# Optimization experiments

Measured on AMD Instinct MI355X. Metric: run time of the kernel, lower is better.

Reference implementation:

```python
import jax, jax.numpy as jnp
import numpy as np

S, B, H = 2048, 2, 2048
NH = 16
HD = H // NH  # 128
ROPE_BASE = 10000.0


def _rope_cos_sin(seq_len, dim, dtype):
    inv_freq = 1.0 / (ROPE_BASE ** (jnp.arange(0, dim, 2, dtype=jnp.float32) / dim))
    t = jnp.arange(seq_len, dtype=jnp.float32)
    freqs = jnp.outer(t, inv_freq)            # [S, dim/2]
    emb = jnp.concatenate([freqs, freqs], -1)  # [S, dim]
    return jnp.cos(emb).astype(dtype), jnp.sin(emb).astype(dtype)


def _rotate_half(x):
    x1, x2 = jnp.split(x, 2, axis=-1)
    return jnp.concatenate([-x2, x1], axis=-1)


def setup_inputs() -> dict:
    key = jax.random.key(0)
    k1, k2, k3 = jax.random.split(key, 3)
    hidden_states = jax.random.normal(k1, (S, B, H), dtype=jnp.float32)
    w_qkv = jax.random.normal(k2, (3 * H, H), dtype=jnp.float32) * (1.0 / np.sqrt(H))
    w_out = jax.random.normal(k3, (H, H), dtype=jnp.float32) * (1.0 / np.sqrt(H))
    return {"hidden_states": hidden_states, "w_qkv": w_qkv, "w_out": w_out}


def reference(hidden_states, w_qkv, w_out):
    seq_len, batch, _ = hidden_states.shape
    # QKV projection (nn.Linear: x @ W^T), bias=False
    qkv = jnp.einsum('sbh,oh->sbo', hidden_states, w_qkv)
    qkv = qkv.reshape(seq_len, batch, 3, NH, HD)
    q, k, v = qkv[:, :, 0], qkv[:, :, 1], qkv[:, :, 2]  # [S, B, NH, HD]

    cos, sin = _rope_cos_sin(seq_len, HD, hidden_states.dtype)
    cos = cos[:, None, None, :]
    sin = sin[:, None, None, :]
    q = q * cos + _rotate_half(q) * sin
    k = k * cos + _rotate_half(k) * sin

    # [S, B, NH, HD] -> [B, NH, S, HD]
    q = q.transpose(1, 2, 0, 3)
    k = k.transpose(1, 2, 0, 3)
    v = v.transpose(1, 2, 0, 3)

    scale = 1.0 / np.sqrt(HD)
    scores = jnp.einsum('bhqd,bhkd->bhqk', q, k) * scale
    causal = jnp.tril(jnp.ones((seq_len, seq_len), dtype=bool))
    scores = jnp.where(causal, scores, jnp.finfo(scores.dtype).min)
    probs = jax.nn.softmax(scores, axis=-1)
    attn = jnp.einsum('bhqk,bhkd->bhqd', probs, v)  # [B, NH, S, HD]

    # [B, NH, S, HD] -> [S, B, NH*HD]
    out = attn.transpose(2, 0, 1, 3).reshape(seq_len, batch, -1)
    out = jnp.einsum('sbh,oh->sbo', out, w_out)
    return out
```

## Files before the change

### kernel.cpp

```cpp
#include <hip/hip_runtime.h>
#include <hip/hip_bf16.h>

typedef __attribute__((ext_vector_type(8))) short bf16x8;
typedef __attribute__((ext_vector_type(8))) short s16x8;
typedef __attribute__((ext_vector_type(4))) float f32x4;
typedef __attribute__((ext_vector_type(4))) int i32x4;
typedef __attribute__((ext_vector_type(2))) unsigned u32x2;

#define SEQ 2048
#define BATCH 2
#define HID 2048
#define NH 16
#define HD 128
#define QKVN 6144
#define QKN 4096

static __device__ __forceinline__ short f2bf(float f) {
    union { float f; unsigned u; } v; v.f = f;
    unsigned r = (v.u + 0x7FFFu + ((v.u >> 16) & 1u)) >> 16;
    return (short)r;
}

static __device__ __forceinline__ void gload_lds16(const short* g, short* l) {
    __builtin_amdgcn_global_load_lds((const __attribute__((address_space(1))) void*)g,
                                     (__attribute__((address_space(3))) void*)l, 16, 0, 0);
}

static __device__ __forceinline__ void cvt_body(const float* in, short* out, int i) {
    f32x4 a = *(const f32x4*)(in + (size_t)i * 8);
    f32x4 b = *(const f32x4*)(in + (size_t)i * 8 + 4);
    s16x8 o = { f2bf(a.x), f2bf(a.y), f2bf(a.z), f2bf(a.w),
                f2bf(b.x), f2bf(b.y), f2bf(b.z), f2bf(b.w) };
    *(s16x8*)(out + (size_t)i * 8) = o;
}

__global__ void cvt_kernel(const float* __restrict__ in, short* __restrict__ out, int n8) {
    const int i = blockIdx.x * 256 + threadIdx.x;
    if (i >= n8) return;
    cvt_body(in, out, i);
}

__global__ void cvt2_kernel(const float* __restrict__ inA, short* __restrict__ outA,
                            const float* __restrict__ inB, short* __restrict__ outB) {
    const int bid = blockIdx.x;
    if (bid < 4096) cvt_body(inA, outA, bid * 256 + threadIdx.x);
    else            cvt_body(inB, outB, (bid - 4096) * 256 + threadIdx.x);
}

#define G128_STAGE_A(BUF, HA, KK) do { \
    const short* _s = ((HA) ? aS1 : aS0) + (size_t)(KK) * 64; \
    short* _d = lds + (BUF) * 16384 + (HA) * 8192 + w * 512; \
    gload_lds16(_s, _d); \
    gload_lds16(_s + (size_t)128 * K, _d + 4096); \
} while (0)

#define G128_STAGE_B(BUF, HB, KK) do { \
    const short* _s = ((HB) ? bS1 : bS0) + (size_t)(KK) * 64; \
    short* _d = lds + 32768 + (BUF) * 8192 + (HB) * 4096 + w * 512; \
    gload_lds16(_s, _d); \
} while (0)

#define G128_LOAD_A(HA) do { \
    const short* _p = lds + bufR * 16384 + (HA) * 8192; \
    _Pragma("unroll") \
    for (int mm = 0; mm < 2; ++mm) { \
        aR[mm][0] = *(const bf16x8*)(_p + aOff0 + mm * 1024); \
        aR[mm][1] = *(const bf16x8*)(_p + aOff1 + mm * 1024); \
    } \
} while (0)

#define G128_LOAD_B(HB) do { \
    const short* _p = lds + 32768 + bufR * 8192 + (HB) * 4096; \
    _Pragma("unroll") \
    for (int nn = 0; nn < 2; ++nn) { \
        bR[(HB) * 2 + nn][0] = *(const bf16x8*)(_p + bOff0 + nn * 2048); \
        bR[(HB) * 2 + nn][1] = *(const bf16x8*)(_p + bOff1 + nn * 2048); \
    } \
} while (0)

#define G128_MFMA(HA, HB) do { \
    _Pragma("unroll") \
    for (int mm = 0; mm < 2; ++mm) { \
        _Pragma("unroll") \
        for (int nn = 0; nn < 2; ++nn) { \
            f32x4 _c = acc[(HA) * 2 + mm][(HB) * 2 + nn]; \
            _c = __builtin_amdgcn_mfma_f32_16x16x32_bf16(aR[mm][0], bR[(HB) * 2 + nn][0], _c, 0, 0, 0); \
            _c = __builtin_amdgcn_mfma_f32_16x16x32_bf16(aR[mm][1], bR[(HB) * 2 + nn][1], _c, 0, 0, 0); \
            acc[(HA) * 2 + mm][(HB) * 2 + nn] = _c; \
        } \
    } \
} while (0)

template<int MODE>
__global__ __launch_bounds__(512, 2)
void gemm128n(const short* __restrict__ A, const short* __restrict__ B,
              void* __restrict__ Cp, short* __restrict__ vTp, int N, int K) {
    __shared__ short lds[49152];

    const int tid = threadIdx.x;
    const int mBase = blockIdx.y * 256;
    const int nBase = blockIdx.x * 128;
    const int w = tid >> 6, lane = tid & 63, quad = lane >> 4, l15 = lane & 15;
    const int wm = w >> 1, wn = w & 1;

    const int kcol = 8 * ((tid & 7) ^ ((tid >> 3) & 7));
    const int srow = ((tid >> 3) & 15) + (tid >> 7) * 32;
    const short* aS0 = A + (size_t)(mBase + srow) * K + kcol;
    const short* aS1 = aS0 + (size_t)16 * K;
    const short* bS0 = B + (size_t)(nBase + srow) * K + kcol;
    const short* bS1 = bS0 + (size_t)16 * K;

    const int cs0 = (quad * 8) ^ ((l15 & 7) << 3);
    const int aOff0 = (l15 + wm * 32) * 64 + cs0;
    const int aOff1 = aOff0 ^ 32;
    const int bOff0 = (l15 + wn * 16) * 64 + cs0;
    const int bOff1 = bOff0 ^ 32;

    const int NK = K >> 6;
    f32x4 acc[4][4] = {};
    bf16x8 aR[2][2], bR[4][2];

    G128_STAGE_A(0, 0, 0); G128_STAGE_B(0, 0, 0); G128_STAGE_B(0, 1, 0); G128_STAGE_A(0, 1, 0);
    G128_STAGE_A(1, 0, 1); G128_STAGE_B(1, 0, 1); G128_STAGE_B(1, 1, 1);
    asm volatile("s_waitcnt vmcnt(4)" ::: "memory");
    __builtin_amdgcn_s_barrier();

    int bufR = 0;
    for (int k = 0; k < NK; ++k) {
        const int kk1 = (k + 1 < NK) ? k + 1 : NK - 1;
        const int kk2 = (k + 2 < NK) ? k + 2 : NK - 1;
        G128_LOAD_A(0);
        G128_LOAD_B(0);
        G128_STAGE_A(bufR ^ 1, 1, kk1);
        asm volatile("s_waitcnt lgkmcnt(4)" ::: "memory");
        __builtin_amdgcn_s_barrier();
        asm volatile("s_waitcnt lgkmcnt(0)" ::: "memory");
        __builtin_amdgcn_s_setprio(1);
        G128_MFMA(0, 0);
        __builtin_amdgcn_s_setprio(0);
        __builtin_amdgcn_s_barrier();
        G128_LOAD_B(1);
        G128_STAGE_A(bufR, 0, kk2);
        __builtin_amdgcn_s_barrier();
        asm volatile("s_waitcnt lgkmcnt(0)" ::: "memory");
        __builtin_amdgcn_s_setprio(1);
        G128_MFMA(0, 1);
        __builtin_amdgcn_s_setprio(0);
        __builtin_amdgcn_s_barrier();
        G128_LOAD_A(1);
        G128_STAGE_B(bufR, 0, kk2);
        __builtin_amdgcn_s_barrier();
        asm volatile("s_waitcnt lgkmcnt(0)" ::: "memory");
        __builtin_amdgcn_s_setprio(1);
        G128_MFMA(1, 1);
        __builtin_amdgcn_s_setprio(0);
        __builtin_amdgcn_s_barrier();
        G128_STAGE_B(bufR, 1, kk2);
        asm volatile("s_waitcnt vmcnt(4)" ::: "memory");
        __builtin_amdgcn_s_barrier();
        __builtin_amdgcn_s_setprio(1);
        G128_MFMA(1, 0);
        __builtin_amdgcn_s_setprio(0);
        __builtin_amdgcn_s_barrier();
        bufR ^= 1;
    }
    asm volatile("s_waitcnt vmcnt(0)" ::: "memory");

    if (MODE == 1 && nBase < 4096) {
        const float post = (nBase < 2048) ? 0.08838834764831845f : 1.0f;
        short* C = (short*)Cp;
        #pragma unroll
        for (int af = 0; af < 4; ++af) {
            const int ha = af >> 1, mm = af & 1;
            const int row0 = mBase + wm * 64 + (2 * mm + ha) * 16 + quad * 4;
            #pragma unroll
            for (int hb = 0; hb < 2; ++hb) {
                const int d = wn * 32 + hb * 16 + l15;
                const float inv_freq =
                    __expf(-((float)(2 * d) * (1.0f / 128.0f)) * 9.210340371976184f);
                #pragma unroll
                for (int rp = 0; rp < 2; ++rp) {
                    const int s = (row0 >> 1) + rp;
                    float sn, cs;
                    __sincosf((float)s * inv_freq, &sn, &cs);
                    #pragma unroll
                    for (int rr = 0; rr < 2; ++rr) {
                        const int r = rp * 2 + rr;
                        const float x1 = acc[af][hb * 2 + 0][r];
                        const float x2 = acc[af][hb * 2 + 1][r];
                        const size_t rb = (size_t)(row0 + r) * QKN + nBase + d;
                        C[rb]      = f2bf((x1 * cs - x2 * sn) * post);
                        C[rb + 64] = f2bf((x2 * cs + x1 * sn) * post);
                    }
                }
            }
        }
    } else if (MODE == 1) {
        __builtin_amdgcn_s_barrier();
        #pragma unroll
        for (int af = 0; af < 4; ++af) {
            const int ha = af >> 1, mm = af & 1;
            const int rbase = wm * 64 + (2 * mm + ha) * 16 + quad * 4;
            #pragma unroll
            for (int bg = 0; bg < 4; ++bg) {
                const int hb = bg >> 1, nn = bg & 1;
                const int d = nn * 64 + wn * 32 + hb * 16 + l15;
                #pragma unroll
                for (int bb = 0; bb < 2; ++bb) {
                    const unsigned lo = (unsigned short)f2bf(acc[af][bg][bb]);
                    const unsigned hi = (unsigned short)f2bf(acc[af][bg][bb + 2]);
                    *(unsigned*)&lds[bb * 16896 + d * 132 + (rbase >> 1)] =
                        lo | (hi << 16);
                }
            }
        }
        __syncthreads();
        const int h = (nBase - 4096) >> 7;
        const int s0 = mBase >> 1;
        const int hw = tid >> 5, l5 = tid & 31;
        #pragma unroll
        for (int pass = 0; pass < 16; ++pass) {
            const int rho = pass * 16 + hw;
            const int bb = rho >> 7, dd = rho & 127;
            const u32x2 v2 = *(const u32x2*)&lds[bb * 16896 + dd * 132 + l5 * 4];
            *(u32x2*)&vTp[((size_t)(bb * 16 + h) * 128 + dd) * 2048 + s0 + l5 * 4] = v2;
        }
    } else {
        #pragma unroll
        for (int af = 0; af < 4; ++af) {
            const int ha = af >> 1, mm = af & 1;
            const int row0 = mBase + wm * 64 + (2 * mm + ha) * 16 + quad * 4;
            #pragma unroll
            for (int bg = 0; bg < 4; ++bg) {
                const int hb = bg >> 1, nn = bg & 1;
                const int col = nBase + nn * 64 + wn * 32 + hb * 16 + l15;
                #pragma unroll
                for (int r = 0; r < 4; ++r)
                    ((float*)Cp)[(size_t)(row0 + r) * N + col] = acc[af][bg][r];
            }
        }
    }
}

__global__ __launch_bounds__(256, 2)
void attn_kernel(const short* __restrict__ qkv, const short* __restrict__ vT,
                 short* __restrict__ out) {
    __shared__ short lds[40960];

    const int bx = blockIdx.x;
    const int h = blockIdx.y, b = blockIdx.z;
    const int Aq = (bx & 1) ? (bx >> 1) : (15 - (bx >> 1));
    const int qt = b ? (15 - Aq) : Aq;
    const int tid = threadIdx.x;
    const int w = tid >> 6, lane = tid & 63, quad = lane >> 4, l15 = lane & 15;
    const int bh = b * 16 + h;
    const int cswz = (l15 & 7) << 3;

    bf16x8 aq[2][4];
    #pragma unroll
    for (int m = 0; m < 2; ++m) {
        const short* qbase =
            qkv + (size_t)((qt * 128 + w * 32 + m * 16 + l15) * 2 + b) * QKN + h * 128;
        #pragma unroll
        for (int c = 0; c < 4; ++c)
            aq[m][c] = *(const bf16x8*)(qbase + c * 32 + quad * 8);
    }

    f32x4 oacc[2][8] = {};
    float lpart[2][4] = {};

    const short* kSrc0 = qkv + (size_t)((w * 16 + (lane >> 4)) * 2 + b) * QKN
                       + 2048 + h * 128 + ((lane & 15) ^ (lane >> 4)) * 8;
    const short* kSrc1 = qkv + (size_t)((w * 16 + 4 + (lane >> 4)) * 2 + b) * QKN
                       + 2048 + h * 128 + ((lane & 15) ^ (4 | (lane >> 4))) * 8;
    const short* vSrc = vT + ((size_t)bh * 128 + w * 32 + (lane >> 3)) * 2048
                      + ((lane & 7) ^ ((lane >> 3) & 7)) * 8;
    short* kDst = lds + w * 2048;
    short* vDst = lds + 16384 + w * 2048;

#define STAGE_KV(BUF, KK0) do { \
    const size_t kAdv = (size_t)(KK0) * 2 * QKN; \
    short* _kd = kDst + (BUF) * 8192; \
    short* _vd = vDst + (BUF) * 8192; \
    gload_lds16(kSrc0 + kAdv,                  _kd); \
    gload_lds16(kSrc1 + kAdv,                  _kd + 512); \
    gload_lds16(kSrc0 + kAdv + 16 * QKN,       _kd + 1024); \
    gload_lds16(kSrc1 + kAdv + 16 * QKN,       _kd + 1536); \
    gload_lds16(vSrc + (KK0),                  _vd); \
    gload_lds16(vSrc + (KK0) + 8 * 2048,       _vd + 512); \
    gload_lds16(vSrc + (KK0) + 16 * 2048,      _vd + 1024); \
    gload_lds16(vSrc + (KK0) + 24 * 2048,      _vd + 1536); \
} while (0)

    const int nChunks = 2 * qt + 2;

    STAGE_KV(0, 0);
    asm volatile("s_waitcnt vmcnt(0)" ::: "memory");
    __builtin_amdgcn_s_barrier();

    for (int ck = 0; ck < nChunks; ++ck) {
        const int cur = ck & 1;
        const int kk0 = ck * 64;
        if (ck + 1 < nChunks) STAGE_KV(cur ^ 1, kk0 + 64);

        const short* Kc = lds + cur * 8192;
        const short* Vc = lds + 16384 + cur * 8192;
        short* Pw = lds + 32768 + w * 2048;

        f32x4 sc4[2][4] = {};
        #pragma unroll
        for (int c = 0; c < 4; ++c) {
            const int cb = (c * 32 + quad * 8) ^ cswz;
            #pragma unroll
            for (int n = 0; n < 4; ++n) {
                bf16x8 bk = *(const bf16x8*)(Kc + (n * 16 + l15) * 128 + cb);
                sc4[0][n] = __builtin_amdgcn_mfma_f32_16x16x32_bf16(aq[0][c], bk, sc4[0][n], 0, 0, 0);
                sc4[1][n] = __builtin_amdgcn_mfma_f32_16x16x32_bf16(aq[1][c], bk, sc4[1][n], 0, 0, 0);
            }
        }

        const bool diag = (ck >= 2 * qt);
        #pragma unroll
        for (int m = 0; m < 2; ++m) {
            const int rowbase = qt * 128 + w * 32 + m * 16 + quad * 4;
            #pragma unroll
            for (int r = 0; r < 4; ++r) {
                const int prow = m * 16 + quad * 4 + r;
                const int pswz = ((quad * 4 + r) & 7) << 3;
                #pragma unroll
                for (int n = 0; n < 4; ++n) {
                    float sv = sc4[m][n][r];
                    if (diag && (kk0 + n * 16 + l15 > rowbase + r)) sv = -1e30f;
                    const float p = __expf(sv);
                    lpart[m][r] += p;
                    Pw[prow * 64 + ((n * 16 + l15) ^ pswz)] = f2bf(p);
                }
            }
        }

        #pragma unroll
        for (int kp2 = 0; kp2 < 2; ++kp2) {
            const int cb = (kp2 * 32 + quad * 8) ^ cswz;
            bf16x8 ap0 = *(const bf16x8*)(Pw + l15 * 64 + cb);
            bf16x8 ap1 = *(const bf16x8*)(Pw + (16 + l15) * 64 + cb);
            #pragma unroll
            for (int dt = 0; dt < 8; ++dt) {
                bf16x8 bv = *(const bf16x8*)(Vc + (dt * 16 + l15) * 64 + cb);
                oacc[0][dt] = __builtin_amdgcn_mfma_f32_16x16x32_bf16(ap0, bv, oacc[0][dt], 0, 0, 0);
                oacc[1][dt] = __builtin_amdgcn_mfma_f32_16x16x32_bf16(ap1, bv, oacc[1][dt], 0, 0, 0);
            }
        }

        asm volatile("s_waitcnt vmcnt(0)" ::: "memory");
        __builtin_amdgcn_s_barrier();
    }
#undef STAGE_KV

    #pragma unroll
    for (int m = 0; m < 2; ++m) {
        const int rowbase = qt * 128 + w * 32 + m * 16 + quad * 4;
        #pragma unroll
        for (int r = 0; r < 4; ++r) {
            float l = lpart[m][r];
            #pragma unroll
            for (int off = 1; off < 16; off <<= 1)
                l += __shfl_xor(l, off);
            const float inv_l = 1.0f / l;
            const size_t obase = (size_t)((rowbase + r) * 2 + b) * HID + h * 128;
            #pragma unroll
            for (int dt = 0; dt < 8; ++dt)
                out[obase + dt * 16 + l15] = f2bf(oacc[m][dt][r] * inv_l);
        }
    }
}

extern "C" void kernel_launch(void* const* d_in, const int* in_sizes, int n_in,
                              void* d_out, int out_size, void* d_ws, size_t ws_size,
                              hipStream_t stream) {
    const float* hidden = (const float*)d_in[0];
    const float* w_qkv  = (const float*)d_in[1];
    const float* w_out  = (const float*)d_in[2];
    float* out = (float*)d_out;

    short* qkv     = (short*)d_ws;
    short* attnb   = qkv + (size_t)4096 * QKN;
    short* wqkv_bf = attnb + (size_t)4096 * HID;
    short* wout_bf = wqkv_bf;
    short* hbf     = wqkv_bf + (size_t)QKVN * HID;
    short* vT      = hbf + (size_t)4096 * HID;

    dim3 blk(256);
    cvt2_kernel<<<dim3(4096 + 6144), blk, 0, stream>>>(hidden, hbf, w_qkv, wqkv_bf);
    gemm128n<1><<<dim3(QKVN / 128, 4096 / 256), dim3(512), 0, stream>>>(
        hbf, wqkv_bf, qkv, vT, QKVN, HID);
    cvt_kernel<<<dim3(2048), blk, 0, stream>>>(w_out, wout_bf, 2048 * 256);
    attn_kernel<<<dim3(SEQ / 128, NH, BATCH), blk, 0, stream>>>(qkv, vT, attnb);
    gemm128n<0><<<dim3(HID / 128, 4096 / 256), dim3(512), 0, stream>>>(
        attnb, wout_bf, out, nullptr, HID, HID);
}
```

Baseline: 345.8 us.

## Transpose QK^T MFMA operands, pack P stores, and pad QK row stride

```diff
diff --git a/kernel.cpp b/kernel.cpp
--- a/kernel.cpp
+++ b/kernel.cpp
@@ -13,7 +13,7 @@
 #define NH 16
 #define HD 128
 #define QKVN 6144
-#define QKN 4096
+#define QKS 4160
 
 static __device__ __forceinline__ short f2bf(float f) {
     union { float f; unsigned u; } v; v.f = f;
@@ -188,7 +188,7 @@
                         const int r = rp * 2 + rr;
                         const float x1 = acc[af][hb * 2 + 0][r];
                         const float x2 = acc[af][hb * 2 + 1][r];
-                        const size_t rb = (size_t)(row0 + r) * QKN + nBase + d;
+                        const size_t rb = (size_t)(row0 + r) * QKS + nBase + d;
                         C[rb]      = f2bf((x1 * cs - x2 * sn) * post);
                         C[rb + 64] = f2bf((x2 * cs + x1 * sn) * post);
                     }
@@ -260,18 +260,18 @@
     #pragma unroll
     for (int m = 0; m < 2; ++m) {
         const short* qbase =
-            qkv + (size_t)((qt * 128 + w * 32 + m * 16 + l15) * 2 + b) * QKN + h * 128;
+            qkv + (size_t)((qt * 128 + w * 32 + m * 16 + l15) * 2 + b) * QKS + h * 128;
         #pragma unroll
         for (int c = 0; c < 4; ++c)
             aq[m][c] = *(const bf16x8*)(qbase + c * 32 + quad * 8);
     }
 
     f32x4 oacc[2][8] = {};
-    float lpart[2][4] = {};
-
-    const short* kSrc0 = qkv + (size_t)((w * 16 + (lane >> 4)) * 2 + b) * QKN
+    float lpart[2] = {};
+
+    const short* kSrc0 = qkv + (size_t)((w * 16 + (lane >> 4)) * 2 + b) * QKS
                        + 2048 + h * 128 + ((lane & 15) ^ (lane >> 4)) * 8;
-    const short* kSrc1 = qkv + (size_t)((w * 16 + 4 + (lane >> 4)) * 2 + b) * QKN
+    const short* kSrc1 = qkv + (size_t)((w * 16 + 4 + (lane >> 4)) * 2 + b) * QKS
                        + 2048 + h * 128 + ((lane & 15) ^ (4 | (lane >> 4))) * 8;
     const short* vSrc = vT + ((size_t)bh * 128 + w * 32 + (lane >> 3)) * 2048
                       + ((lane & 7) ^ ((lane >> 3) & 7)) * 8;
@@ -279,13 +279,13 @@
     short* vDst = lds + 16384 + w * 2048;
 
 #define STAGE_KV(BUF, KK0) do { \
-    const size_t kAdv = (size_t)(KK0) * 2 * QKN; \
+    const size_t kAdv = (size_t)(KK0) * 2 * QKS; \
     short* _kd = kDst + (BUF) * 8192; \
     short* _vd = vDst + (BUF) * 8192; \
     gload_lds16(kSrc0 + kAdv,                  _kd); \
     gload_lds16(kSrc1 + kAdv,                  _kd + 512); \
-    gload_lds16(kSrc0 + kAdv + 16 * QKN,       _kd + 1024); \
-    gload_lds16(kSrc1 + kAdv + 16 * QKN,       _kd + 1536); \
+    gload_lds16(kSrc0 + kAdv + 16 * QKS,       _kd + 1024); \
+    gload_lds16(kSrc1 + kAdv + 16 * QKS,       _kd + 1536); \
     gload_lds16(vSrc + (KK0),                  _vd); \
     gload_lds16(vSrc + (KK0) + 8 * 2048,       _vd + 512); \
     gload_lds16(vSrc + (KK0) + 16 * 2048,      _vd + 1024); \
@@ -307,34 +307,40 @@
         const short* Vc = lds + 16384 + cur * 8192;
         short* Pw = lds + 32768 + w * 2048;
 
-        f32x4 sc4[2][4] = {};
+        f32x4 sc4[4][2] = {};
         #pragma unroll
         for (int c = 0; c < 4; ++c) {
             const int cb = (c * 32 + quad * 8) ^ cswz;
             #pragma unroll
-            for (int n = 0; n < 4; ++n) {
-                bf16x8 bk = *(const bf16x8*)(Kc + (n * 16 + l15) * 128 + cb);
-                sc4[0][n] = __builtin_amdgcn_mfma_f32_16x16x32_bf16(aq[0][c], bk, sc4[0][n], 0, 0, 0);
-                sc4[1][n] = __builtin_amdgcn_mfma_f32_16x16x32_bf16(aq[1][c], bk, sc4[1][n], 0, 0, 0);
+            for (int kc = 0; kc < 4; ++kc) {
+                bf16x8 ak = *(const bf16x8*)(Kc + (kc * 16 + l15) * 128 + cb);
+                sc4[kc][0] = __builtin_amdgcn_mfma_f32_16x16x32_bf16(ak, aq[0][c], sc4[kc][0], 0, 0, 0);
+                sc4[kc][1] = __builtin_amdgcn_mfma_f32_16x16x32_bf16(ak, aq[1][c], sc4[kc][1], 0, 0, 0);
             }
         }
 
         const bool diag = (ck >= 2 * qt);
-        #pragma unroll
-        for (int m = 0; m < 2; ++m) {
-            const int rowbase = qt * 128 + w * 32 + m * 16 + quad * 4;
-            #pragma unroll
-            for (int r = 0; r < 4; ++r) {
-                const int prow = m * 16 + quad * 4 + r;
-                const int pswz = ((quad * 4 + r) & 7) << 3;
+        const int dq = qt * 128 + w * 32 + l15 - kk0;
+        #pragma unroll
+        for (int kc = 0; kc < 4; ++kc) {
+            #pragma unroll
+            for (int qn = 0; qn < 2; ++qn) {
+                float p[4];
                 #pragma unroll
-                for (int n = 0; n < 4; ++n) {
-                    float sv = sc4[m][n][r];
-                    if (diag && (kk0 + n * 16 + l15 > rowbase + r)) sv = -1e30f;
-                    const float p = __expf(sv);
-                    lpart[m][r] += p;
-                    Pw[prow * 64 + ((n * 16 + l15) ^ pswz)] = f2bf(p);
+                for (int r = 0; r < 4; ++r) {
+                    float sv = sc4[kc][qn][r];
+                    if (diag && (kc * 16 + quad * 4 + r > dq + qn * 16)) sv = -1e30f;
+                    p[r] = __expf(sv);
+                    lpart[qn] += p[r];
                 }
+                const unsigned pk0 = (unsigned short)f2bf(p[0])
+                                   | ((unsigned)(unsigned short)f2bf(p[1]) << 16);
+                const unsigned pk1 = (unsigned short)f2bf(p[2])
+                                   | ((unsigned)(unsigned short)f2bf(p[3]) << 16);
+                unsigned* pp = (unsigned*)&Pw[(qn * 16 + l15) * 64
+                                              + ((kc * 16 + quad * 4) ^ cswz)];
+                pp[0] = pk0;
+                pp[1] = pk1;
             }
         }
 
@@ -357,16 +363,18 @@
 #undef STAGE_KV
 
     #pragma unroll
+    for (int qn = 0; qn < 2; ++qn) {
+        lpart[qn] += __shfl_xor(lpart[qn], 16);
+        lpart[qn] += __shfl_xor(lpart[qn], 32);
+    }
+    #pragma unroll
     for (int m = 0; m < 2; ++m) {
-        const int rowbase = qt * 128 + w * 32 + m * 16 + quad * 4;
         #pragma unroll
         for (int r = 0; r < 4; ++r) {
-            float l = lpart[m][r];
-            #pragma unroll
-            for (int off = 1; off < 16; off <<= 1)
-                l += __shfl_xor(l, off);
+            const int row = qt * 128 + w * 32 + m * 16 + quad * 4 + r;
+            const float l = __shfl(lpart[m], quad * 4 + r);
             const float inv_l = 1.0f / l;
-            const size_t obase = (size_t)((rowbase + r) * 2 + b) * HID + h * 128;
+            const size_t obase = (size_t)(row * 2 + b) * HID + h * 128;
             #pragma unroll
             for (int dt = 0; dt < 8; ++dt)
                 out[obase + dt * 16 + l15] = f2bf(oacc[m][dt][r] * inv_l);
@@ -383,10 +391,10 @@
     float* out = (float*)d_out;
 
     short* qkv     = (short*)d_ws;
-    short* attnb   = qkv + (size_t)4096 * QKN;
-    short* wqkv_bf = attnb + (size_t)4096 * HID;
+    short* wqkv_bf = qkv + (size_t)4096 * QKS;
     short* wout_bf = wqkv_bf;
     short* hbf     = wqkv_bf + (size_t)QKVN * HID;
+    short* attnb   = hbf;
     short* vT      = hbf + (size_t)4096 * HID;
 
     dim3 blk(256);
```

Measured after the change: 338.4 us. 2.1% less time.
